# Optimization experiments

Hardware: AMD Instinct MI355X
Metric: run time of the kernel (lower is better)

The kernel has to match this reference:

```python
import jax, jax.numpy as jnp
import numpy as np
from jax import lax

V, D, H, K, B, T = 32000, 300, 300, 9, 64, 512


def _lstm_dir(x, w_ih, w_hh, b_ih, b_hh, h0, c0):
    # x: [B, T, D]; torch gate order: i, f, g, o
    def step(carry, xt):
        h, c = carry
        gates = xt @ w_ih.T + h @ w_hh.T + b_ih + b_hh  # [B, 4H]
        i, f, g, o = jnp.split(gates, 4, axis=-1)
        i, f, o = jax.nn.sigmoid(i), jax.nn.sigmoid(f), jax.nn.sigmoid(o)
        g = jnp.tanh(g)
        c = f * c + i * g
        h = o * jnp.tanh(c)
        return (h, c), h

    xs = jnp.transpose(x, (1, 0, 2))  # [T, B, D]
    _, hs = lax.scan(step, (h0, c0), xs)
    return jnp.transpose(hs, (1, 0, 2))  # [B, T, H]


def _emissions(tokens, emb, w_ih_f, w_hh_f, b_ih_f, b_hh_f,
               w_ih_b, w_hh_b, b_ih_b, b_hh_b, h0, c0, w_out, b_out):
    x = emb[tokens]  # [B, T, D]
    hf = _lstm_dir(x, w_ih_f, w_hh_f, b_ih_f, b_hh_f, h0[0], c0[0])
    hb = _lstm_dir(jnp.flip(x, axis=1), w_ih_b, w_hh_b, b_ih_b, b_hh_b, h0[1], c0[1])
    hb = jnp.flip(hb, axis=1)
    out = jnp.concatenate([hf, hb], axis=-1)  # [B, T, 2H]
    return out @ w_out.T + b_out  # [B, T, K]


def _crf_nll(emissions, tags, mask, start_t, end_t, trans):
    # torchcrf: -sum_b log p(tags | emissions)
    e = jnp.transpose(emissions, (1, 0, 2))  # [T, B, K]
    tg = tags.T                               # [T, B]
    m = mask.T.astype(emissions.dtype)        # [T, B]
    bidx = jnp.arange(tags.shape[0])
    # numerator: gold path score
    num = start_t[tg[0]] + e[0][bidx, tg[0]]
    def nstep(carry, inp):
        et, tt, tp, mt = inp
        return carry + (trans[tp, tt] + et[bidx, tt]) * mt, None
    num, _ = lax.scan(nstep, num, (e[1:], tg[1:], tg[:-1], m[1:]))
    last_idx = mask.sum(axis=1).astype(jnp.int32) - 1
    last_tags = tags[bidx, last_idx]
    num = num + end_t[last_tags]
    # denominator: forward algorithm
    alpha = start_t + e[0]  # [B, K]
    def dstep(alpha, inp):
        et, mt = inp
        nxt = jax.scipy.special.logsumexp(alpha[:, :, None] + trans[None], axis=1) + et
        return jnp.where(mt[:, None] > 0, nxt, alpha), None
    alpha, _ = lax.scan(dstep, alpha, (e[1:], m[1:]))
    den = jax.scipy.special.logsumexp(alpha + end_t, axis=1)
    return -jnp.sum(num - den)


def _viterbi(emissions, mask, start_t, end_t, trans):
    e = jnp.transpose(emissions, (1, 0, 2))  # [T, B, K]
    m = mask.T                               # [T, B]
    score = start_t + e[0]                   # [B, K]
    def fstep(score, inp):
        et, mt = inp
        br = score[:, :, None] + trans[None]  # [B, K_prev, K_next]
        best = br.max(axis=1)
        idx = br.argmax(axis=1).astype(jnp.int32)  # [B, K]
        new = best + et
        return jnp.where(mt[:, None], new, score), idx
    score, history = lax.scan(fstep, score, (e[1:], m[1:]))  # history: [T-1, B, K]
    score = score + end_t
    last = jnp.argmax(score, axis=-1).astype(jnp.int32)  # [B]
    def bstep(tag, inp):
        idx_t, mt = inp
        prev = jnp.take_along_axis(idx_t, tag[:, None], axis=1)[:, 0]
        tag = jnp.where(mt, prev, tag)
        return tag, tag
    _, tags_rev = lax.scan(bstep, last, (history, m[1:]), reverse=True)  # [T-1, B]
    path = jnp.concatenate([tags_rev, last[None]], axis=0)  # [T, B]
    return path.T  # [B, T]


def setup_inputs() -> dict:
    key = jax.random.key(0)
    ks = jax.random.split(key, 20)
    s = 0.1
    emb = jax.random.normal(ks[0], (V, D), jnp.float32) * s
    emb = emb.at[0].set(0.0)  # padding_idx row
    inp = {
        "tokens": jax.random.randint(ks[1], (B, T), 0, V, jnp.int32),
        "tags": jax.random.randint(ks[2], (B, T), 0, K, jnp.int32),
        "mask": jnp.ones((B, T), jnp.bool_),
        "emb": emb,
        "w_ih_f": jax.random.normal(ks[3], (4 * H, D), jnp.float32) * s,
        "w_hh_f": jax.random.normal(ks[4], (4 * H, H), jnp.float32) * s,
        "b_ih_f": jax.random.normal(ks[5], (4 * H,), jnp.float32) * s,
        "b_hh_f": jax.random.normal(ks[6], (4 * H,), jnp.float32) * s,
        "w_ih_b": jax.random.normal(ks[7], (4 * H, D), jnp.float32) * s,
        "w_hh_b": jax.random.normal(ks[8], (4 * H, H), jnp.float32) * s,
        "b_ih_b": jax.random.normal(ks[9], (4 * H,), jnp.float32) * s,
        "b_hh_b": jax.random.normal(ks[10], (4 * H,), jnp.float32) * s,
        "h0": jax.random.normal(ks[11], (2, B, H), jnp.float32),
        "c0": jax.random.normal(ks[12], (2, B, H), jnp.float32),
        "w_out": jax.random.normal(ks[13], (K, 2 * H), jnp.float32) * s,
        "b_out": jax.random.normal(ks[14], (K,), jnp.float32) * s,
        "start_t": jax.random.normal(ks[15], (K,), jnp.float32) * s,
        "end_t": jax.random.normal(ks[16], (K,), jnp.float32) * s,
        "trans": jax.random.normal(ks[17], (K, K), jnp.float32) * s,
    }
    return inp


def reference(tokens, tags, mask, emb, w_ih_f, w_hh_f, b_ih_f, b_hh_f,
              w_ih_b, w_hh_b, b_ih_b, b_hh_b, h0, c0, w_out, b_out,
              start_t, end_t, trans):
    feats = _emissions(tokens, emb, w_ih_f, w_hh_f, b_ih_f, b_hh_f,
                       w_ih_b, w_hh_b, b_ih_b, b_hh_b, h0, c0, w_out, b_out)
    paths = _viterbi(feats, mask, start_t, end_t, trans)
    loss = _crf_nll(feats, tags, mask, start_t, end_t, trans)
    return paths, loss
```

## Files before the change

### kernel.cpp

```cpp
#include <hip/hip_runtime.h>
#include <math.h>

#define NV 32000
#define ND 300
#define NH 300
#define NK 9
#define NB 64
#define NT 512

typedef short bf16x8 __attribute__((ext_vector_type(8)));
typedef float f32x4  __attribute__((ext_vector_type(4)));

__device__ inline short bf16r(float x) {
    return (short)((__float_as_uint(x) + 0x8000u) >> 16);
}

#define WB_OFF   0ull
#define WB_F     768000ull
#define E_OFF    (WB_OFF + WB_F)
#define E_SZ     ((unsigned long long)NT*NB*NK)
#define CBUF_OFF (E_OFF + E_SZ)
#define CBUF_SZ  (2ull*NB*NH)
#define HSLOT_OFF (CBUF_OFF + CBUF_SZ)
#define HSLOT_SZ  (2ull*2*NB*NH)
#define XP_OFF   (HSLOT_OFF + HSLOT_SZ)
#define XPC_SZ   (2ull*64*1200*64)

__global__ __launch_bounds__(256) void k_wcvt(
    const float* __restrict__ wihf, const float* __restrict__ wihb,
    const float* __restrict__ whhf, const float* __restrict__ whhb,
    short* __restrict__ dst)
{
    int i = blockIdx.x*256 + threadIdx.x;
    if (i >= 1536000) return;
    int d  = i / 384000;
    int r2 = i % 384000;
    int j  = r2 / 320, k = r2 % 320;
    const float* src = (d == 0) ? wihf : (d == 1) ? wihb : (d == 2) ? whhf : whhb;
    float v = (k < 300) ? src[(size_t)j*300 + k] : 0.f;
    dst[i] = bf16r(v);
}

__global__ __launch_bounds__(256) void k_xproj(
    const int* __restrict__ tokens, const float* __restrict__ emb,
    const short* __restrict__ wb16,
    const float* __restrict__ bif, const float* __restrict__ bhf,
    const float* __restrict__ bib, const float* __restrict__ bhb,
    float* __restrict__ xpc, int chunk)
{
    const int tid = threadIdx.x;
    const int w  = tid >> 6, L = tid & 63;
    const int lm = L & 15, lq = L >> 4;
    const int dir = blockIdx.z;
    const int m0 = blockIdx.x*128 + w*32;
    const int n0 = blockIdx.y*80;
    const int tbase = dir ? (448 - chunk*64) : (chunk*64);

    const float* arow[2];
#pragma unroll
    for (int mi = 0; mi < 2; ++mi) {
        int m = m0 + mi*16 + lm;
        int b = m >> 6, lt = m & 63;
        arow[mi] = emb + (size_t)tokens[b*512 + tbase + lt] * 300;
    }
    const short* brow[5];
#pragma unroll
    for (int ni = 0; ni < 5; ++ni) {
        int j = n0 + ni*16 + lm;
        brow[ni] = wb16 + ((size_t)dir*1200 + j)*320;
    }

    f32x4 acc[2][5];
#pragma unroll
    for (int mi = 0; mi < 2; ++mi)
#pragma unroll
        for (int ni = 0; ni < 5; ++ni)
#pragma unroll
            for (int r = 0; r < 4; ++r) acc[mi][ni][r] = 0.f;

    const float4 z4 = make_float4(0.f,0.f,0.f,0.f);
    for (int k0 = 0; k0 < 320; k0 += 32) {
        const int kk = k0 + lq*8;
        bf16x8 af[2], bf[5];
#pragma unroll
        for (int mi = 0; mi < 2; ++mi) {
            float4 f1 = (kk   < 300) ? *(const float4*)(arow[mi] + kk)     : z4;
            float4 f2 = (kk+4 < 300) ? *(const float4*)(arow[mi] + kk + 4) : z4;
            af[mi][0]=bf16r(f1.x); af[mi][1]=bf16r(f1.y); af[mi][2]=bf16r(f1.z); af[mi][3]=bf16r(f1.w);
            af[mi][4]=bf16r(f2.x); af[mi][5]=bf16r(f2.y); af[mi][6]=bf16r(f2.z); af[mi][7]=bf16r(f2.w);
        }
#pragma unroll
        for (int ni = 0; ni < 5; ++ni)
            bf[ni] = *(const bf16x8*)(brow[ni] + kk);
#pragma unroll
        for (int mi = 0; mi < 2; ++mi)
#pragma unroll
            for (int ni = 0; ni < 5; ++ni)
                acc[mi][ni] = __builtin_amdgcn_mfma_f32_16x16x32_bf16(
                                  af[mi], bf[ni], acc[mi][ni], 0, 0, 0);
    }

#pragma unroll
    for (int ni = 0; ni < 5; ++ni) {
        int j = n0 + ni*16 + lm;
        int g = j/300, rr = j%300;
        int slc = rr/20, ul = rr%20;
        float bias = dir ? (bib[j]+bhb[j]) : (bif[j]+bhf[j]);
#pragma unroll
        for (int mi = 0; mi < 2; ++mi) {
#pragma unroll
            for (int r = 0; r < 4; ++r) {
                int m = m0 + mi*16 + lq*4 + r;
                int b = m >> 6, lt = m & 63;
                int sp = dir ? (63 - lt) : lt;
                size_t idx = ((((size_t)dir*64 + sp)*8 + (b>>3))*15 + slc)*640
                           + (size_t)(b&7)*80 + g*20 + ul;
                xpc[idx] = acc[mi][ni][r] + bias;
            }
        }
    }
}

__global__ __launch_bounds__(256) void k_rnn(
    const float* __restrict__ xpc,
    const short* __restrict__ whh16,
    const float* __restrict__ h0,
    unsigned* hslot, float* __restrict__ cbuf,
    float* __restrict__ ev, const float* __restrict__ wout,
    int s_begin, int s_count, int full)
{
    extern __shared__ char lds_pad[];
    __shared__ __align__(16) short h_sh16[16*328];
    __shared__ __align__(16) float xp_sh[640];
    __shared__ __align__(16) float gates_sh[80*9];
    __shared__ __align__(16) float wo_sh[180];
    __shared__ __align__(16) float hloc[160];
    (void)lds_pad;

    const int tid = threadIdx.x;
    const int wv  = tid >> 6, L = tid & 63;
    const int lm  = L & 15, lq = L >> 4;
    const int dir = blockIdx.x / 120;
    const int rem = blockIdx.x % 120;
    const int sl  = rem / 8;
    const int gb  = rem % 8;
    const int u0  = sl * 20;

    const int tb = (wv == 0) ? 0 : (wv + 1);
    const int tn = (wv == 0) ? 2 : 1;

    bf16x8 A[2][10];
#pragma unroll 2
    for (int mt = 0; mt < 2; ++mt) {
        if (mt < tn) {
            int r = (tb + mt)*16 + lm;
            int grow = (r/20)*300 + u0 + (r%20);
            const short* wr = whh16 + ((size_t)dir*1200 + grow)*320;
#pragma unroll
            for (int ks = 0; ks < 10; ++ks)
                A[mt][ks] = *(const bf16x8*)(wr + ks*32 + lq*8);
        }
    }
    if (tid < 180) wo_sh[tid] = wout[(tid/20)*600 + dir*300 + u0 + (tid%20)];

    for (int i = tid; i < 16*328; i += 256) h_sh16[i] = 0;

    const bool isPW = (tid < 160);
    const int bl_p = tid/20, lu_p = tid%20;
    float c_reg = 0.f;
    if (isPW) c_reg = cbuf[((size_t)dir*NB + gb*8 + bl_p)*NH + u0 + lu_p];

    __syncthreads();

    for (int s = s_begin; s < s_begin + s_count; ++s) {
        const int t = dir ? (511 - s) : s;
        const float* xb; int sp;
        if (full) { xb = xpc + (size_t)(s >> 6)*XPC_SZ; sp = s & 63; }
        else      { xb = xpc;                            sp = s - s_begin; }

        unsigned vb[10];
        unsigned* hsrc = hslot + (((size_t)(s & 1)*2 + dir)*NB + gb*8)*NH;
        if (s > 0 && tid < 240) {
#pragma unroll
            for (int j = 0; j < 10; ++j) {
                int i = tid + 256*j;
                if (i < 2400)
                    vb[j] = __hip_atomic_load(hsrc + i, __ATOMIC_RELAXED,
                                              __HIP_MEMORY_SCOPE_AGENT);
            }
        }

        {
            const float* xsrc = xb + ((((size_t)dir*64 + sp)*8 + gb)*15 + sl)*640;
            if (tid < 160) *(float4*)(&xp_sh[tid*4]) = *(const float4*)(xsrc + tid*4);
        }

        if (s == 0) {
            const float* h0p = h0 + ((size_t)dir*NB + gb*8)*NH;
            for (int i = tid; i < 2400; i += 256)
                h_sh16[(i/300)*328 + (i%300)] = bf16r(h0p[i]);
        } else if (tid < 240) {
            const unsigned tg = (unsigned)s & 0xFFFFu;
            bool ok = false;
            while (!ok) {
                ok = true;
#pragma unroll
                for (int j = 0; j < 10; ++j) {
                    int i = tid + 256*j;
                    if (i < 2400 && (vb[j] >> 16) != tg) {
                        ok = false;
                        vb[j] = __hip_atomic_load(hsrc + i, __ATOMIC_RELAXED,
                                                  __HIP_MEMORY_SCOPE_AGENT);
                    }
                }
            }
#pragma unroll
            for (int j = 0; j < 10; ++j) {
                int i = tid + 256*j;
                if (i < 2400)
                    h_sh16[(i/300)*328 + (i%300)] = (short)(vb[j] & 0xFFFFu);
            }
        }
        __syncthreads();

        {
            bf16x8 Bf[10];
#pragma unroll
            for (int ks = 0; ks < 10; ++ks)
                Bf[ks] = *(const bf16x8*)(h_sh16 + lm*328 + ks*32 + lq*8);
            f32x4 acc[2];
#pragma unroll 2
            for (int mt = 0; mt < 2; ++mt) {
                if (mt < tn) {
#pragma unroll
                    for (int r = 0; r < 4; ++r) acc[mt][r] = 0.f;
#pragma unroll
                    for (int ks = 0; ks < 10; ++ks)
                        acc[mt] = __builtin_amdgcn_mfma_f32_16x16x32_bf16(
                                      A[mt][ks], Bf[ks], acc[mt], 0, 0, 0);
                    if (lm < 8) {
#pragma unroll
                        for (int r = 0; r < 4; ++r)
                            gates_sh[((tb+mt)*16 + lq*4 + r)*9 + lm] = acc[mt][r];
                    }
                }
            }
        }
        __syncthreads();

        if (isPW) {
            float G[4];
#pragma unroll
            for (int g = 0; g < 4; ++g)
                G[g] = xp_sh[bl_p*80 + g*20 + lu_p] + gates_sh[(g*20 + lu_p)*9 + bl_p];
            float ig = 1.f/(1.f+__expf(-G[0]));
            float fg = 1.f/(1.f+__expf(-G[1]));
            float gg = tanhf(G[2]);
            float og = 1.f/(1.f+__expf(-G[3]));
            c_reg = fg*c_reg + ig*gg;
            float h = og*tanhf(c_reg);
            hloc[bl_p*20 + lu_p] = h;
            unsigned hb = (__float_as_uint(h) + 0x8000u) >> 16;
            unsigned pk = (((unsigned)(s+1) & 0xFFFFu) << 16) | hb;
            __hip_atomic_store(
                &hslot[(((size_t)((s+1)&1)*2 + dir)*NB + gb*8 + bl_p)*NH + u0 + lu_p],
                pk, __ATOMIC_RELAXED, __HIP_MEMORY_SCOPE_AGENT);
        }
        __syncthreads();

        if (tid < 72) {
            int b = tid/9, k = tid%9;
            float a = 0.f;
#pragma unroll
            for (int u = 0; u < 20; ++u) a += hloc[b*20+u]*wo_sh[k*20+u];
            atomicAdd(&ev[((size_t)t*NB + gb*8 + b)*NK + k], a);
        }
    }

    if (isPW) cbuf[((size_t)dir*NB + gb*8 + bl_p)*NH + u0 + lu_p] = c_reg;
}

__global__ __launch_bounds__(64) void k_crf(
    const float* __restrict__ ev, const int* __restrict__ tags,
    const float* __restrict__ start_t, const float* __restrict__ end_t,
    const float* __restrict__ trans, const float* __restrict__ bout,
    float* __restrict__ out)
{
    __shared__ __align__(16) float ex_sh[32];
    __shared__ int hist_sh[511*NK];
    const int b = blockIdx.x, ln = threadIdx.x;

    float part = 0.f;
    for (int t = ln; t < NT; t += 64) {
        int tc = tags[b*NT + t];
        float e = ev[((size_t)t*NB + b)*NK + tc] + bout[tc];
        float pre = (t == 0) ? start_t[tc] : trans[tags[b*NT + t - 1]*9 + tc];
        part += pre + e;
    }
    if (ln == 63) part += end_t[tags[b*NT + NT - 1]];
#pragma unroll
    for (int off = 32; off > 0; off >>= 1)
        part += __shfl_down(part, off, 64);
    const float num = part;

    const bool isA = (ln < 9);
    const bool isV = (ln >= 16 && ln < 25);
    const int kc = isV ? (ln - 16) : (isA ? ln : 0);
    float Tc[9];
#pragma unroll
    for (int kp = 0; kp < 9; ++kp) {
        float v = trans[kp*9 + kc];
        Tc[kp] = isA ? __expf(v) : v;
    }
    const float bo = bout[kc];
    float init = start_t[kc] + ev[(size_t)b*NK + kc] + bo;
    if (isA | isV) ex_sh[ln] = init;
    const int base = (ln < 16) ? 0 : 16;

    float etn = ev[((size_t)1*NB + b)*NK + kc] + bo;

    for (int t = 1; t < NT; ++t) {
        float et = etn;
        if (t + 1 < NT) etn = ev[((size_t)(t+1)*NB + b)*NK + kc] + bo;

        float4 s0 = *(const float4*)(&ex_sh[base]);
        float4 s1 = *(const float4*)(&ex_sh[base + 4]);
        float  a8 = ex_sh[base + 8];
        float a0=s0.x,a1=s0.y,a2=s0.z,a3=s0.w,a4=s1.x,a5=s1.y,a6=s1.z,a7=s1.w;

        float outv = 0.f;
        if (isA) {
            float M = fmaxf(fmaxf(fmaxf(a0,a1),fmaxf(a2,a3)),
                            fmaxf(fmaxf(a4,a5),fmaxf(a6,a7)));
            M = fmaxf(M, a8);
            float s =        __expf(a0-M)*Tc[0];
            s = fmaf(__expf(a1-M), Tc[1], s);
            s = fmaf(__expf(a2-M), Tc[2], s);
            s = fmaf(__expf(a3-M), Tc[3], s);
            s = fmaf(__expf(a4-M), Tc[4], s);
            s = fmaf(__expf(a5-M), Tc[5], s);
            s = fmaf(__expf(a6-M), Tc[6], s);
            s = fmaf(__expf(a7-M), Tc[7], s);
            s = fmaf(__expf(a8-M), Tc[8], s);
            outv = M + __logf(s) + et;
        } else if (isV) {
            float bv = a0 + Tc[0]; int arg = 0;
            float v;
            v = a1+Tc[1]; if (v > bv) { bv = v; arg = 1; }
            v = a2+Tc[2]; if (v > bv) { bv = v; arg = 2; }
            v = a3+Tc[3]; if (v > bv) { bv = v; arg = 3; }
            v = a4+Tc[4]; if (v > bv) { bv = v; arg = 4; }
            v = a5+Tc[5]; if (v > bv) { bv = v; arg = 5; }
            v = a6+Tc[6]; if (v > bv) { bv = v; arg = 6; }
            v = a7+Tc[7]; if (v > bv) { bv = v; arg = 7; }
            v = a8+Tc[8]; if (v > bv) { bv = v; arg = 8; }
            outv = bv + et;
            hist_sh[(t-1)*NK + (ln-16)] = arg;
        }
        if (isA | isV) ex_sh[ln] = outv;
    }

    if (ln == 0) {
        float M = -1e30f;
#pragma unroll
        for (int k = 0; k < 9; ++k) M = fmaxf(M, ex_sh[k] + end_t[k]);
        float ls = 0.f;
#pragma unroll
        for (int k = 0; k < 9; ++k) ls += __expf(ex_sh[k] + end_t[k] - M);
        float den = M + __logf(ls);
        atomicAdd(out + NB*NT, den - num);

        float best = -1e30f; int last = 0;
#pragma unroll
        for (int k = 0; k < 9; ++k) {
            float v = ex_sh[16 + k] + end_t[k];
            if (v > best) { best = v; last = k; }
        }
        int* pout = (int*)out;
        pout[b*NT + NT - 1] = last;
        for (int i = NT - 2; i >= 0; --i) {
            last = hist_sh[i*NK + last];
            pout[b*NT + i] = last;
        }
    }
}

extern "C" void kernel_launch(void* const* d_in, const int* in_sizes, int n_in,
                              void* d_out, int out_size, void* d_ws, size_t ws_size,
                              hipStream_t stream)
{
    (void)in_sizes; (void)n_in;

    const int*   tokens = (const int*)  d_in[0];
    const int*   tags   = (const int*)  d_in[1];
    const float* emb    = (const float*)d_in[3];
    const float* wihf   = (const float*)d_in[4];
    const float* whhf   = (const float*)d_in[5];
    const float* bihf   = (const float*)d_in[6];
    const float* bhhf   = (const float*)d_in[7];
    const float* wihb   = (const float*)d_in[8];
    const float* whhb   = (const float*)d_in[9];
    const float* bib    = (const float*)d_in[10];
    const float* bhhb   = (const float*)d_in[11];
    const float* h0     = (const float*)d_in[12];
    const float* c0     = (const float*)d_in[13];
    const float* wout   = (const float*)d_in[14];
    const float* bout   = (const float*)d_in[15];
    const float* startt = (const float*)d_in[16];
    const float* endt   = (const float*)d_in[17];
    const float* trans  = (const float*)d_in[18];

    float* ws    = (float*)d_ws;
    short* wb16  = (short*)(ws + WB_OFF);
    short* whh16 = wb16 + 768000;
    float* evp   = ws + E_OFF;
    float* cbuf  = ws + CBUF_OFF;
    unsigned* hslot = (unsigned*)(ws + HSLOT_OFF);
    float* xp    = ws + XP_OFF;
    float* out   = (float*)d_out;

    const size_t need_full = (XP_OFF + 8ull*XPC_SZ) * 4ull;
    const bool full = (ws_size >= need_full);

    (void)hipMemsetAsync(d_out, 0, (size_t)out_size * sizeof(float), stream);
    (void)hipMemsetAsync(evp, 0, (size_t)E_SZ * sizeof(float), stream);
    (void)hipMemcpyAsync(cbuf, c0, 2ull*NB*NH*sizeof(float), hipMemcpyDeviceToDevice, stream);

    k_wcvt<<<6000, 256, 0, stream>>>(wihf, wihb, whhf, whhb, wb16);

    if (full) {
        for (int c = 0; c < 8; ++c)
            k_xproj<<<dim3(32, 15, 2), 256, 0, stream>>>(
                tokens, emb, wb16, bihf, bhhf, bib, bhhb, xp + (size_t)c*XPC_SZ, c);
        k_rnn<<<240, 256, 81920, stream>>>(
            xp, whh16, h0, hslot, cbuf, evp, wout, 0, 512, 1);
    } else {
        for (int c = 0; c < 8; ++c) {
            k_xproj<<<dim3(32, 15, 2), 256, 0, stream>>>(
                tokens, emb, wb16, bihf, bhhf, bib, bhhb, xp, c);
            k_rnn<<<240, 256, 81920, stream>>>(
                xp, whh16, h0, hslot, cbuf, evp, wout, c*64, 64, 0);
        }
    }
    k_crf<<<64, 64, 0, stream>>>(evp, tags, startt, endt, trans, bout, out);
}
```

Measured before the change: 1.967 ms.

## Prefetch xproj, lighten barriers, split MFMA chains, fast tanh, parallel Viterbi backtrace

The recurrent kernel now prefetches the next step's input-projection slice into registers, replaces __syncthreads with an LDS-only wait plus s_barrier, splits the MFMA accumulation into two independent chains, uses an exp-based tanh, and moves the hloc write after the atomic h store. The CRF kernel's serial Viterbi backtrace is parallelized into 14 chunks using composed pointer maps computed by 126 threads. The goal is to shorten the per-step critical path of the latency-bound recurrence and the serial backtrace tail. Risks include the lighter barrier not covering global-memory ordering, and fast tanh overflowing for large inputs (exp→inf still yields 1, so it is likely safe).

```diff
diff --git a/kernel.cpp b/kernel.cpp
--- a/kernel.cpp
+++ b/kernel.cpp
@@ -13,6 +13,17 @@
 
 __device__ inline short bf16r(float x) {
     return (short)((__float_as_uint(x) + 0x8000u) >> 16);
+}
+
+__device__ inline float tanh_fast(float x) {
+    float e2 = __expf(2.f * x);
+    return 1.f - 2.f / (e2 + 1.f);
+}
+
+__device__ inline void bar_lds() {
+    asm volatile("s_waitcnt lgkmcnt(0)" ::: "memory");
+    __builtin_amdgcn_s_barrier();
+    asm volatile("" ::: "memory");
 }
 
 #define WB_OFF   0ull
@@ -170,13 +181,19 @@
     float c_reg = 0.f;
     if (isPW) c_reg = cbuf[((size_t)dir*NB + gb*8 + bl_p)*NH + u0 + lu_p];
 
-    __syncthreads();
-
-    for (int s = s_begin; s < s_begin + s_count; ++s) {
-        const int t = dir ? (511 - s) : s;
+    auto xaddr = [&](int s) -> const float* {
         const float* xb; int sp;
         if (full) { xb = xpc + (size_t)(s >> 6)*XPC_SZ; sp = s & 63; }
         else      { xb = xpc;                            sp = s - s_begin; }
+        return xb + ((((size_t)dir*64 + sp)*8 + gb)*15 + sl)*640 + (size_t)tid*4;
+    };
+    float4 xpr;
+    if (tid < 160) xpr = *(const float4*)xaddr(s_begin);
+
+    bar_lds();
+
+    for (int s = s_begin; s < s_begin + s_count; ++s) {
+        const int t = dir ? (511 - s) : s;
 
         unsigned vb[10];
         unsigned* hsrc = hslot + (((size_t)(s & 1)*2 + dir)*NB + gb*8)*NH;
@@ -190,10 +207,9 @@
             }
         }
 
-        {
-            const float* xsrc = xb + ((((size_t)dir*64 + sp)*8 + gb)*15 + sl)*640;
-            if (tid < 160) *(float4*)(&xp_sh[tid*4]) = *(const float4*)(xsrc + tid*4);
-        }
+        if (tid < 160) *(float4*)(&xp_sh[tid*4]) = xpr;
+        if (tid < 160 && (s + 1) < s_begin + s_count)
+            xpr = *(const float4*)xaddr(s + 1);
 
         if (s == 0) {
             const float* h0p = h0 + ((size_t)dir*NB + gb*8)*NH;
@@ -221,32 +237,36 @@
                     h_sh16[(i/300)*328 + (i%300)] = (short)(vb[j] & 0xFFFFu);
             }
         }
-        __syncthreads();
+        bar_lds();
 
         {
             bf16x8 Bf[10];
 #pragma unroll
             for (int ks = 0; ks < 10; ++ks)
                 Bf[ks] = *(const bf16x8*)(h_sh16 + lm*328 + ks*32 + lq*8);
-            f32x4 acc[2];
+            f32x4 acc0, acc1;
 #pragma unroll 2
             for (int mt = 0; mt < 2; ++mt) {
                 if (mt < tn) {
 #pragma unroll
-                    for (int r = 0; r < 4; ++r) acc[mt][r] = 0.f;
-#pragma unroll
-                    for (int ks = 0; ks < 10; ++ks)
-                        acc[mt] = __builtin_amdgcn_mfma_f32_16x16x32_bf16(
-                                      A[mt][ks], Bf[ks], acc[mt], 0, 0, 0);
+                    for (int r = 0; r < 4; ++r) { acc0[r] = 0.f; acc1[r] = 0.f; }
+#pragma unroll
+                    for (int ks = 0; ks < 5; ++ks)
+                        acc0 = __builtin_amdgcn_mfma_f32_16x16x32_bf16(
+                                   A[mt][ks], Bf[ks], acc0, 0, 0, 0);
+#pragma unroll
+                    for (int ks = 5; ks < 10; ++ks)
+                        acc1 = __builtin_amdgcn_mfma_f32_16x16x32_bf16(
+                                   A[mt][ks], Bf[ks], acc1, 0, 0, 0);
                     if (lm < 8) {
 #pragma unroll
                         for (int r = 0; r < 4; ++r)
-                            gates_sh[((tb+mt)*16 + lq*4 + r)*9 + lm] = acc[mt][r];
+                            gates_sh[((tb+mt)*16 + lq*4 + r)*9 + lm] = acc0[r] + acc1[r];
                     }
                 }
             }
         }
-        __syncthreads();
+        bar_lds();
 
         if (isPW) {
             float G[4];
@@ -255,18 +275,18 @@
                 G[g] = xp_sh[bl_p*80 + g*20 + lu_p] + gates_sh[(g*20 + lu_p)*9 + bl_p];
             float ig = 1.f/(1.f+__expf(-G[0]));
             float fg = 1.f/(1.f+__expf(-G[1]));
-            float gg = tanhf(G[2]);
+            float gg = tanh_fast(G[2]);
             float og = 1.f/(1.f+__expf(-G[3]));
             c_reg = fg*c_reg + ig*gg;
-            float h = og*tanhf(c_reg);
-            hloc[bl_p*20 + lu_p] = h;
+            float h = og*tanh_fast(c_reg);
             unsigned hb = (__float_as_uint(h) + 0x8000u) >> 16;
             unsigned pk = (((unsigned)(s+1) & 0xFFFFu) << 16) | hb;
             __hip_atomic_store(
                 &hslot[(((size_t)((s+1)&1)*2 + dir)*NB + gb*8 + bl_p)*NH + u0 + lu_p],
                 pk, __ATOMIC_RELAXED, __HIP_MEMORY_SCOPE_AGENT);
-        }
-        __syncthreads();
+            hloc[bl_p*20 + lu_p] = h;
+        }
+        bar_lds();
 
         if (tid < 72) {
             int b = tid/9, k = tid%9;
@@ -280,7 +300,10 @@
     if (isPW) cbuf[((size_t)dir*NB + gb*8 + bl_p)*NH + u0 + lu_p] = c_reg;
 }
 
-__global__ __launch_bounds__(64) void k_crf(
+#define BT_C 14
+#define BT_L 37
+
+__global__ __launch_bounds__(128) void k_crf(
     const float* __restrict__ ev, const int* __restrict__ tags,
     const float* __restrict__ start_t, const float* __restrict__ end_t,
     const float* __restrict__ trans, const float* __restrict__ bout,
@@ -288,101 +311,133 @@
 {
     __shared__ __align__(16) float ex_sh[32];
     __shared__ int hist_sh[511*NK];
-    const int b = blockIdx.x, ln = threadIdx.x;
-
-    float part = 0.f;
-    for (int t = ln; t < NT; t += 64) {
-        int tc = tags[b*NT + t];
-        float e = ev[((size_t)t*NB + b)*NK + tc] + bout[tc];
-        float pre = (t == 0) ? start_t[tc] : trans[tags[b*NT + t - 1]*9 + tc];
-        part += pre + e;
-    }
-    if (ln == 63) part += end_t[tags[b*NT + NT - 1]];
-#pragma unroll
-    for (int off = 32; off > 0; off >>= 1)
-        part += __shfl_down(part, off, 64);
-    const float num = part;
-
-    const bool isA = (ln < 9);
-    const bool isV = (ln >= 16 && ln < 25);
-    const int kc = isV ? (ln - 16) : (isA ? ln : 0);
-    float Tc[9];
-#pragma unroll
-    for (int kp = 0; kp < 9; ++kp) {
-        float v = trans[kp*9 + kc];
-        Tc[kp] = isA ? __expf(v) : v;
-    }
-    const float bo = bout[kc];
-    float init = start_t[kc] + ev[(size_t)b*NK + kc] + bo;
-    if (isA | isV) ex_sh[ln] = init;
-    const int base = (ln < 16) ? 0 : 16;
-
-    float etn = ev[((size_t)1*NB + b)*NK + kc] + bo;
-
-    for (int t = 1; t < NT; ++t) {
-        float et = etn;
-        if (t + 1 < NT) etn = ev[((size_t)(t+1)*NB + b)*NK + kc] + bo;
-
-        float4 s0 = *(const float4*)(&ex_sh[base]);
-        float4 s1 = *(const float4*)(&ex_sh[base + 4]);
-        float  a8 = ex_sh[base + 8];
-        float a0=s0.x,a1=s0.y,a2=s0.z,a3=s0.w,a4=s1.x,a5=s1.y,a6=s1.z,a7=s1.w;
-
-        float outv = 0.f;
-        if (isA) {
-            float M = fmaxf(fmaxf(fmaxf(a0,a1),fmaxf(a2,a3)),
-                            fmaxf(fmaxf(a4,a5),fmaxf(a6,a7)));
-            M = fmaxf(M, a8);
-            float s =        __expf(a0-M)*Tc[0];
-            s = fmaf(__expf(a1-M), Tc[1], s);
-            s = fmaf(__expf(a2-M), Tc[2], s);
-            s = fmaf(__expf(a3-M), Tc[3], s);
-            s = fmaf(__expf(a4-M), Tc[4], s);
-            s = fmaf(__expf(a5-M), Tc[5], s);
-            s = fmaf(__expf(a6-M), Tc[6], s);
-            s = fmaf(__expf(a7-M), Tc[7], s);
-            s = fmaf(__expf(a8-M), Tc[8], s);
-            outv = M + __logf(s) + et;
-        } else if (isV) {
-            float bv = a0 + Tc[0]; int arg = 0;
-            float v;
-            v = a1+Tc[1]; if (v > bv) { bv = v; arg = 1; }
-            v = a2+Tc[2]; if (v > bv) { bv = v; arg = 2; }
-            v = a3+Tc[3]; if (v > bv) { bv = v; arg = 3; }
-            v = a4+Tc[4]; if (v > bv) { bv = v; arg = 4; }
-            v = a5+Tc[5]; if (v > bv) { bv = v; arg = 5; }
-            v = a6+Tc[6]; if (v > bv) { bv = v; arg = 6; }
-            v = a7+Tc[7]; if (v > bv) { bv = v; arg = 7; }
-            v = a8+Tc[8]; if (v > bv) { bv = v; arg = 8; }
-            outv = bv + et;
-            hist_sh[(t-1)*NK + (ln-16)] = arg;
-        }
-        if (isA | isV) ex_sh[ln] = outv;
-    }
-
-    if (ln == 0) {
-        float M = -1e30f;
-#pragma unroll
-        for (int k = 0; k < 9; ++k) M = fmaxf(M, ex_sh[k] + end_t[k]);
-        float ls = 0.f;
-#pragma unroll
-        for (int k = 0; k < 9; ++k) ls += __expf(ex_sh[k] + end_t[k] - M);
-        float den = M + __logf(ls);
-        atomicAdd(out + NB*NT, den - num);
-
-        float best = -1e30f; int last = 0;
-#pragma unroll
-        for (int k = 0; k < 9; ++k) {
-            float v = ex_sh[16 + k] + end_t[k];
-            if (v > best) { best = v; last = k; }
-        }
-        int* pout = (int*)out;
-        pout[b*NT + NT - 1] = last;
-        for (int i = NT - 2; i >= 0; --i) {
-            last = hist_sh[i*NK + last];
-            pout[b*NT + i] = last;
-        }
-    }
+    __shared__ int fmap[BT_C*NK];
+    __shared__ int entry_sh[BT_C];
+    __shared__ int last_sh;
+
+    const int b = blockIdx.x, tid = threadIdx.x, ln = tid & 63;
+
+    if (tid < 64) {
+        float part = 0.f;
+        for (int t = ln; t < NT; t += 64) {
+            int tc = tags[b*NT + t];
+            float e = ev[((size_t)t*NB + b)*NK + tc] + bout[tc];
+            float pre = (t == 0) ? start_t[tc] : trans[tags[b*NT + t - 1]*9 + tc];
+            part += pre + e;
+        }
+        if (ln == 63) part += end_t[tags[b*NT + NT - 1]];
+#pragma unroll
+        for (int off = 32; off > 0; off >>= 1)
+            part += __shfl_down(part, off, 64);
+        const float num = part;
+
+        const bool isA = (ln < 9);
+        const bool isV = (ln >= 16 && ln < 25);
+        const int kc = isV ? (ln - 16) : (isA ? ln : 0);
+        float Tc[9];
+#pragma unroll
+        for (int kp = 0; kp < 9; ++kp) {
+            float v = trans[kp*9 + kc];
+            Tc[kp] = isA ? __expf(v) : v;
+        }
+        const float bo = bout[kc];
+        float init = start_t[kc] + ev[(size_t)b*NK + kc] + bo;
+        if (isA | isV) ex_sh[ln] = init;
+        const int base = (ln < 16) ? 0 : 16;
+
+        float etn = ev[((size_t)1*NB + b)*NK + kc] + bo;
+
+        for (int t = 1; t < NT; ++t) {
+            float et = etn;
+            if (t + 1 < NT) etn = ev[((size_t)(t+1)*NB + b)*NK + kc] + bo;
+
+            float4 s0 = *(const float4*)(&ex_sh[base]);
+            float4 s1 = *(const float4*)(&ex_sh[base + 4]);
+            float  a8 = ex_sh[base + 8];
+            float a0=s0.x,a1=s0.y,a2=s0.z,a3=s0.w,a4=s1.x,a5=s1.y,a6=s1.z,a7=s1.w;
+
+            float outv = 0.f;
+            if (isA) {
+                float M = fmaxf(fmaxf(fmaxf(a0,a1),fmaxf(a2,a3)),
+                                fmaxf(fmaxf(a4,a5),fmaxf(a6,a7)));
+                M = fmaxf(M, a8);
+                float s =        __expf(a0-M)*Tc[0];
+                s = fmaf(__expf(a1-M), Tc[1], s);
+                s = fmaf(__expf(a2-M), Tc[2], s);
+                s = fmaf(__expf(a3-M), Tc[3], s);
+                s = fmaf(__expf(a4-M), Tc[4], s);
+                s = fmaf(__expf(a5-M), Tc[5], s);
+                s = fmaf(__expf(a6-M), Tc[6], s);
+                s = fmaf(__expf(a7-M), Tc[7], s);
+                s = fmaf(__expf(a8-M), Tc[8], s);
+                outv = M + __logf(s) + et;
+            } else if (isV) {
+                float bv = a0 + Tc[0]; int arg = 0;
+                float v;
+                v = a1+Tc[1]; if (v > bv) { bv = v; arg = 1; }
+                v = a2+Tc[2]; if (v > bv) { bv = v; arg = 2; }
+                v = a3+Tc[3]; if (v > bv) { bv = v; arg = 3; }
+                v = a4+Tc[4]; if (v > bv) { bv = v; arg = 4; }
+                v = a5+Tc[5]; if (v > bv) { bv = v; arg = 5; }
+                v = a6+Tc[6]; if (v > bv) { bv = v; arg = 6; }
+                v = a7+Tc[7]; if (v > bv) { bv = v; arg = 7; }
+                v = a8+Tc[8]; if (v > bv) { bv = v; arg = 8; }
+                outv = bv + et;
+                hist_sh[(t-1)*NK + (ln-16)] = arg;
+            }
+            if (isA | isV) ex_sh[ln] = outv;
+        }
+
+        if (ln == 0) {
+            float M = -1e30f;
+#pragma unroll
+            for (int k = 0; k < 9; ++k) M = fmaxf(M, ex_sh[k] + end_t[k]);
+            float ls = 0.f;
+#pragma unroll
+            for (int k = 0; k < 9; ++k) ls += __expf(ex_sh[k] + end_t[k] - M);
+            float den = M + __logf(ls);
+            atomicAdd(out + NB*NT, den - num);
+
+            float best = -1e30f; int last = 0;
+#pragma unroll
+            for (int k = 0; k < 9; ++k) {
+                float v = ex_sh[16 + k] + end_t[k];
+                if (v > best) { best = v; last = k; }
+            }
+            last_sh = last;
+        }
+    }
+
+    __syncthreads();
+
+    if (tid < BT_C*NK) {
+        int c = tid / NK, s = tid % NK;
+        int lo = c*BT_L, hi = min(511, lo + BT_L);
+        int pos = s;
+        for (int i = hi - 1; i >= lo; --i) pos = hist_sh[i*NK + pos];
+        fmap[c*NK + s] = pos;
+    }
+    __syncthreads();
+    if (tid == 0) {
+        int e = last_sh;
+        entry_sh[BT_C-1] = e;
+        for (int c = BT_C - 2; c >= 0; --c) {
+            e = fmap[(c+1)*NK + e];
+            entry_sh[c] = e;
+        }
+    }
+    __syncthreads();
+    int* pout = (int*)out;
+    if (tid < BT_C) {
+        int c = tid;
+        int lo = c*BT_L, hi = min(511, lo + BT_L);
+        int pos = entry_sh[c];
+        for (int i = hi - 1; i >= lo; --i) {
+            pos = hist_sh[i*NK + pos];
+            pout[b*NT + i] = pos;
+        }
+    }
+    if (tid == 0) pout[b*NT + NT - 1] = last_sh;
 }
 
 extern "C" void kernel_launch(void* const* d_in, const int* in_sizes, int n_in,
@@ -442,5 +497,5 @@
                 xp, whh16, h0, hslot, cbuf, evp, wout, c*64, 64, 0);
         }
     }
-    k_crf<<<64, 64, 0, stream>>>(evp, tags, startt, endt, trans, bout, out);
-}
+    k_crf<<<64, 128, 0, stream>>>(evp, tags, startt, endt, trans, bout, out);
+}
```

New measurement: 2.059 ms. +4.7%, slower.
